# Kernel tuning notes

Hardware: AMD Instinct MI355X
Metric: run time of the kernel (lower is better)

Reference implementation:

```python
import jax, jax.numpy as jnp
import numpy as np

USERNUM = 100_000
ITEMNUM = 50_000
EMBED_DIM = 64
N_INTERACTIONS = 2_000_000
NUM_LAYERS = 3
BATCH = 4096


def setup_inputs() -> dict:
    rng = np.random.default_rng(0)
    # random bipartite interactions: users 1..USERNUM, items 1..ITEMNUM
    u = rng.integers(1, USERNUM + 1, N_INTERACTIONS)
    it = rng.integers(1, ITEMNUM + 1, N_INTERACTIONS)
    # node ids: user k -> k, item j -> USERNUM + j (matches build_graph)
    rows = np.concatenate([u, USERNUM + it]).astype(np.int32)
    cols = np.concatenate([USERNUM + it, u]).astype(np.int32)
    n_nodes = USERNUM + ITEMNUM + 1
    # symmetric normalization D^-1/2 A D^-1/2 (duplicate edges sum, as in scipy COO)
    deg = np.bincount(rows, minlength=n_nodes).astype(np.float32)
    d_inv_sqrt = np.where(deg > 0, deg ** -0.5, 0.0).astype(np.float32)
    vals = (d_inv_sqrt[rows] * d_inv_sqrt[cols]).astype(np.float32)

    key = jax.random.key(0)
    k1, k2, k3, k4, k5 = jax.random.split(key, 5)
    # xavier_normal init: std = sqrt(2 / (fan_in + fan_out))
    u_std = np.sqrt(2.0 / (USERNUM + 1 + EMBED_DIM)).astype(np.float32)
    i_std = np.sqrt(2.0 / (ITEMNUM + 1 + EMBED_DIM)).astype(np.float32)
    user_table = jax.random.normal(k1, (USERNUM + 1, EMBED_DIM), jnp.float32) * u_std
    item_table = jax.random.normal(k2, (ITEMNUM + 1, EMBED_DIM), jnp.float32) * i_std

    user_ids = jax.random.randint(k3, (BATCH,), 0, USERNUM + 1)
    pos_seqs = jax.random.randint(k4, (BATCH,), 1, ITEMNUM + 1)
    neg_seqs = jax.random.randint(k5, (BATCH,), 1, ITEMNUM + 1)

    return {
        "user_table": user_table,
        "item_table": item_table,
        "vals": jnp.asarray(vals),
        "rows": jnp.asarray(rows),
        "cols": jnp.asarray(cols),
        "user_ids": user_ids,
        "pos_seqs": pos_seqs,
        "neg_seqs": neg_seqs,
    }


def reference(user_table, item_table, vals, rows, cols, user_ids, pos_seqs, neg_seqs):
    usernum = user_table.shape[0] - 1
    itemnum = item_table.shape[0] - 1
    n_nodes = usernum + itemnum + 1

    # ego embeddings: users 0..usernum, items 1..itemnum (skip item padding row)
    x = jnp.concatenate([user_table, item_table[1:]], axis=0)  # [n_nodes, D]

    # LightGCN propagation: x_{l+1} = A_norm @ x_l (SpMM via gather + segment_sum),
    # layer combination = mean over layers 0..NUM_LAYERS
    acc = x
    for _ in range(NUM_LAYERS):
        msgs = vals[:, None] * x[cols]              # [nnz, D]
        x = jax.ops.segment_sum(msgs, rows, num_segments=n_nodes)
        acc = acc + x
    all_emb = acc / (NUM_LAYERS + 1)

    uidx = jnp.clip(user_ids, 0, usernum)
    pidx = usernum + jnp.clip(pos_seqs, 1, itemnum)  # item j lives at row usernum + j
    nidx = usernum + jnp.clip(neg_seqs, 1, itemnum)

    u_emb = all_emb[uidx]
    pos_logits = jnp.sum(u_emb * all_emb[pidx], axis=-1)
    neg_logits = jnp.sum(u_emb * all_emb[nidx], axis=-1)
    return pos_logits, neg_logits
```

## Files before the change

### kernel.cpp

```cpp
#include <hip/hip_runtime.h>
#include <hip/hip_fp16.h>
#include <cstdint>
#include <cstddef>


typedef __attribute__((ext_vector_type(8))) _Float16 half8;

#define NB_SHIFT 8
#define BCAP 16000
#define P1_SRC 4096
#define P1_DIM 512

__global__ __launch_bounds__(P1_DIM) void partition_kernel(
    const int* __restrict__ rows, const int* __restrict__ cols,
    int* __restrict__ bucket_cursor, int* __restrict__ tmp,
    int M , int nb) {
    __shared__ int            lhist[1024];
    __shared__ int            loff[1024];
    __shared__ int            ldelta[1024];
    __shared__ int            wsum[8];
    __shared__ int            stage[2 * P1_SRC];
    __shared__ unsigned short bstage[2 * P1_SRC];
    int t = threadIdx.x;
    int lane = t & 63, wv = t >> 6;
    int base     = blockIdx.x * P1_SRC;
    int cnt_here = min(P1_SRC, M - base);
    int full4    = cnt_here >> 2;
    int rem      = cnt_here & 3;
    for (int i = t; i < 1024; i += P1_DIM) lhist[i] = 0;
    __syncthreads();
    const int4* rows4 = (const int4*)(rows + base);
    const int4* cols4 = (const int4*)(cols + base);
    int4 uu[2], vv[2];
    int  rka[8], rkb[8];
#pragma unroll
    for (int k = 0; k < 2; ++k) {
        int i4 = t + k * P1_DIM;
        if (i4 < full4) {
            uu[k] = rows4[i4];
            vv[k] = cols4[i4];
            int u4[4] = {uu[k].x, uu[k].y, uu[k].z, uu[k].w};
            int v4[4] = {vv[k].x, vv[k].y, vv[k].z, vv[k].w};
#pragma unroll
            for (int e = 0; e < 4; ++e) {
                rka[4 * k + e] = atomicAdd(&lhist[u4[e] >> NB_SHIFT], 1);
                rkb[4 * k + e] = atomicAdd(&lhist[v4[e] >> NB_SHIFT], 1);
            }
        }
    }
    int ur = 0, vr = 0, rkra = 0, rkrb = 0;
    bool has_rem = (t < rem);
    if (has_rem) {
        ur = rows[base + 4 * full4 + t];
        vr = cols[base + 4 * full4 + t];
        rkra = atomicAdd(&lhist[ur >> NB_SHIFT], 1);
        rkrb = atomicAdd(&lhist[vr >> NB_SHIFT], 1);
    }
    __syncthreads();
    int v0 = lhist[2 * t], v1 = lhist[2 * t + 1];
    int ts = v0 + v1;
    int sc = ts;
#pragma unroll
    for (int off = 1; off < 64; off <<= 1) {
        int x = __shfl_up(sc, off);
        if (lane >= off) sc += x;
    }
    if (lane == 63) wsum[wv] = sc;
    __syncthreads();
    int prefix = 0;
#pragma unroll
    for (int k = 0; k < 8; ++k) {
        int s = wsum[k];
        prefix += (k < wv) ? s : 0;
    }
    int run = prefix + sc - ts;
    loff[2 * t]     = run;
    loff[2 * t + 1] = run + v0;
#pragma unroll
    for (int k = 0; k < 2; ++k) {
        int b  = 2 * t + k;
        int vvk = (k == 0) ? v0 : v1;
        if (b < nb && vvk > 0) {
            int old = atomicAdd(&bucket_cursor[b], vvk);
            ldelta[b] = b * BCAP + old - loff[b];
        }
    }
    __syncthreads();
#pragma unroll
    for (int k = 0; k < 2; ++k) {
        int i4 = t + k * P1_DIM;
        if (i4 < full4) {
            int u4[4] = {uu[k].x, uu[k].y, uu[k].z, uu[k].w};
            int v4[4] = {vv[k].x, vv[k].y, vv[k].z, vv[k].w};
#pragma unroll
            for (int e = 0; e < 4; ++e) {
                int ub = u4[e] >> NB_SHIFT;
                int s1 = loff[ub] + rka[4 * k + e];
                stage[s1]  = ((u4[e] & 255) << 18) | v4[e];
                bstage[s1] = (unsigned short)ub;
                int vb = v4[e] >> NB_SHIFT;
                int s2 = loff[vb] + rkb[4 * k + e];
                stage[s2]  = ((v4[e] & 255) << 18) | u4[e];
                bstage[s2] = (unsigned short)vb;
            }
        }
    }
    if (has_rem) {
        int ub = ur >> NB_SHIFT;
        int s1 = loff[ub] + rkra;
        stage[s1]  = ((ur & 255) << 18) | vr;
        bstage[s1] = (unsigned short)ub;
        int vb = vr >> NB_SHIFT;
        int s2 = loff[vb] + rkrb;
        stage[s2]  = ((vr & 255) << 18) | ur;
        bstage[s2] = (unsigned short)vb;
    }
    __syncthreads();
    int total = 2 * cnt_here;
    for (int s = t; s < total; s += P1_DIM) {
        tmp[s + ldelta[bstage[s]]] = stage[s];
    }
}

__global__ __launch_bounds__(256) void finalize_kernel(
    const int* __restrict__ tmp, const int* __restrict__ bcur,
    const float4* __restrict__ ut4, const float4* __restrict__ it4,
    int* __restrict__ row_ptr, float* __restrict__ dis,
    float* __restrict__ dis2, float* __restrict__ invd,
    int* __restrict__ cv, half8* __restrict__ Yh0,
    int usernum, int n_nodes, int nb, int nnz) {
    __shared__ int   rcnt[256];
    __shared__ int   ccur[256];
    __shared__ int   wsum[4];
    __shared__ int   red[256];
    __shared__ float sdis[256];
    int b = blockIdx.x;
    int t = threadIdx.x;
    int lane = t & 63, wv = t >> 6;
    int partial = 0;
    for (int i = t; i < nb; i += 256) {
        int c = bcur[i];
        if (i < b) partial += c;
    }
    red[t] = partial;
    __syncthreads();
    for (int off = 128; off > 0; off >>= 1) {
        if (t < off) red[t] += red[t + off];
        __syncthreads();
    }
    int dbeg  = red[0];
    int count = bcur[b];
    int src   = b * BCAP;
    rcnt[t] = 0;
    __syncthreads();
    for (int i = t; i < count; i += 256) {
        atomicAdd(&rcnt[tmp[src + i] >> 18], 1);
    }
    __syncthreads();
    int v = rcnt[t];
    int sc = v;
#pragma unroll
    for (int off = 1; off < 64; off <<= 1) {
        int x = __shfl_up(sc, off);
        if (lane >= off) sc += x;
    }
    if (lane == 63) wsum[wv] = sc;
    __syncthreads();
    int prefix = 0;
#pragma unroll
    for (int k = 0; k < 4; ++k) {
        int s = wsum[k];
        prefix += (k < wv) ? s : 0;
    }
    int ex = prefix + sc - v;
    ccur[t] = ex;
    int row = (b << NB_SHIFT) + t;
    float dval = 0.0f;
    if (row < n_nodes) {
        row_ptr[row] = dbeg + ex;
        double dv = (double)v;
        dval      = (v > 0) ? (float)(1.0 / sqrt(dv)) : 0.0f;
        dis[row]  = dval;
        dis2[row] = (v > 0) ? (float)(1.0 / dv) : 0.0f;
        invd[row] = (v > 0) ? (float)sqrt(dv) : 0.0f;
    }
    sdis[t] = dval;
    if (b == nb - 1 && t == 0) row_ptr[n_nodes] = nnz;
    __syncthreads();
    for (int i = t; i < count; i += 256) {
        int p  = tmp[src + i];
        int rk = atomicAdd(&ccur[p >> 18], 1);
        cv[dbeg + rk] = p & 0x3FFFF;
    }
    int row0 = b << NB_SHIFT;
    for (int i = t; i < 256 * 8; i += 256) {
        int rl = i >> 3;
        int rg = row0 + rl;
        if (rg < n_nodes) {
            int c = i & 7;
            float d = sdis[rl];
            const float4* srcp = (rg <= usernum)
                ? (ut4 + (size_t)rg * 16 + 2 * c)
                : (it4 + (size_t)(rg - usernum) * 16 + 2 * c);
            float4 a = srcp[0];
            float4 e = srcp[1];
            half8 o;
            o[0] = (_Float16)(d * a.x); o[1] = (_Float16)(d * a.y);
            o[2] = (_Float16)(d * a.z); o[3] = (_Float16)(d * a.w);
            o[4] = (_Float16)(d * e.x); o[5] = (_Float16)(d * e.y);
            o[6] = (_Float16)(d * e.z); o[7] = (_Float16)(d * e.w);
            Yh0[(size_t)rg * 8 + c] = o;
        }
    }
}

__device__ inline float csr_row_sum_h(const _Float16* __restrict__ Yh,
                                      const int* __restrict__ cv,
                                      int beg, int end, int g, int l8,
                                      float one) {
    float acc[8] = {0.f, 0.f, 0.f, 0.f, 0.f, 0.f, 0.f, 0.f};
    const char* Yb = (const char*)Yh;
    const char* cb = (const char*)cv;
    unsigned lo = (unsigned)l8 * 16u;
    int j = beg + g;
    for (; j + 8 < end; j += 16) {
        unsigned c0 = (unsigned)*(const int*)(cb + ((unsigned)j << 2));
        unsigned c1 = (unsigned)*(const int*)(cb + ((unsigned)(j + 8) << 2));
        half8 x0 = *(const half8*)(Yb + (c0 << 7) + lo);
        half8 x1 = *(const half8*)(Yb + (c1 << 7) + lo);
        half8 tt = x0 + x1;
#pragma unroll
        for (int k = 0; k < 8; ++k) {
            acc[k] += one * (float)tt[k];
        }
    }
    if (j < end) {
        unsigned c0 = (unsigned)*(const int*)(cb + ((unsigned)j << 2));
        half8 x0 = *(const half8*)(Yb + (c0 << 7) + lo);
#pragma unroll
        for (int k = 0; k < 8; ++k) {
            acc[k] += one * (float)x0[k];
        }
    }
    bool gb0 = (g & 1) != 0;
    bool gb1 = (g & 2) != 0;
    bool gb2 = (g & 4) != 0;
    float s0 = gb0 ? acc[0] : acc[4];
    float s1 = gb0 ? acc[1] : acc[5];
    float s2 = gb0 ? acc[2] : acc[6];
    float s3 = gb0 ? acc[3] : acc[7];
    float a0 = (gb0 ? acc[4] : acc[0]) + __shfl_xor(s0, 8);
    float a1 = (gb0 ? acc[5] : acc[1]) + __shfl_xor(s1, 8);
    float a2 = (gb0 ? acc[6] : acc[2]) + __shfl_xor(s2, 8);
    float a3 = (gb0 ? acc[7] : acc[3]) + __shfl_xor(s3, 8);
    float t0 = gb1 ? a0 : a2;
    float t1 = gb1 ? a1 : a3;
    float b0 = (gb1 ? a2 : a0) + __shfl_xor(t0, 16);
    float b1 = (gb1 ? a3 : a1) + __shfl_xor(t1, 16);
    float u = gb2 ? b0 : b1;
    float fin = (gb2 ? b1 : b0) + __shfl_xor(u, 32);
    return fin;
}

__device__ inline int lane_dim(int g, int l8) {
    return l8 * 8 + ((g & 1) * 4 + (g & 2) + (g >> 2));
}

__global__ __launch_bounds__(256) void spmm_y_kernel(
    const _Float16* __restrict__ Yin, _Float16* __restrict__ Yout,
    const int* __restrict__ row_ptr, const int* __restrict__ cv,
    const float* __restrict__ dis2, float one, int n_nodes) {
    int wid  = (blockIdx.x * blockDim.x + threadIdx.x) >> 6;
    int lane = threadIdx.x & 63;
    int g = lane >> 3, sub = lane & 7;
    int row = wid * 8 + g;
    bool ok = row < n_nodes;
    int beg = 0, end = 0;
    if (ok) {
        beg = row_ptr[row];
        end = row_ptr[row + 1];
    }
    float d2 = ok ? dis2[row] : 0.0f;
    const char* Yb = (const char*)Yin;
    const char* cb = (const char*)cv;
    unsigned lo = (unsigned)sub * 16u;
    float acc[8] = {0.f, 0.f, 0.f, 0.f, 0.f, 0.f, 0.f, 0.f};
    int len = end - beg;
    int mx = len;
    mx = max(mx, __shfl_xor(mx, 8));
    mx = max(mx, __shfl_xor(mx, 16));
    mx = max(mx, __shfl_xor(mx, 32));
    int iters = (mx + 7) >> 3;
    int j = beg;
    size_t jb = ((size_t)(unsigned)j) << 2;
    int r0 = *(const int*)(cb + jb);
    int r1 = *(const int*)(cb + jb + 4u);
    int r2 = *(const int*)(cb + jb + 8u);
    int r3 = *(const int*)(cb + jb + 12u);
    int r4 = *(const int*)(cb + jb + 16u);
    int r5 = *(const int*)(cb + jb + 20u);
    int r6 = *(const int*)(cb + jb + 24u);
    int r7 = *(const int*)(cb + jb + 28u);
    for (int it = 0; it < iters; ++it) {
        unsigned c0 = (unsigned)((j     < end) ? r0 : 0);
        unsigned c1 = (unsigned)((j + 1 < end) ? r1 : 0);
        unsigned c2 = (unsigned)((j + 2 < end) ? r2 : 0);
        unsigned c3 = (unsigned)((j + 3 < end) ? r3 : 0);
        unsigned c4 = (unsigned)((j + 4 < end) ? r4 : 0);
        unsigned c5 = (unsigned)((j + 5 < end) ? r5 : 0);
        unsigned c6 = (unsigned)((j + 6 < end) ? r6 : 0);
        unsigned c7 = (unsigned)((j + 7 < end) ? r7 : 0);
        half8 x0 = *(const half8*)(Yb + ((size_t)c0 << 7) + lo);
        half8 x1 = *(const half8*)(Yb + ((size_t)c1 << 7) + lo);
        half8 x2 = *(const half8*)(Yb + ((size_t)c2 << 7) + lo);
        half8 x3 = *(const half8*)(Yb + ((size_t)c3 << 7) + lo);
        half8 x4 = *(const half8*)(Yb + ((size_t)c4 << 7) + lo);
        half8 x5 = *(const half8*)(Yb + ((size_t)c5 << 7) + lo);
        half8 x6 = *(const half8*)(Yb + ((size_t)c6 << 7) + lo);
        half8 x7 = *(const half8*)(Yb + ((size_t)c7 << 7) + lo);
        j += 8;
        jb = ((size_t)(unsigned)j) << 2;
        r0 = *(const int*)(cb + jb);
        r1 = *(const int*)(cb + jb + 4u);
        r2 = *(const int*)(cb + jb + 8u);
        r3 = *(const int*)(cb + jb + 12u);
        r4 = *(const int*)(cb + jb + 16u);
        r5 = *(const int*)(cb + jb + 20u);
        r6 = *(const int*)(cb + jb + 24u);
        r7 = *(const int*)(cb + jb + 28u);
        half8 sA = (x0 + x1) + (x2 + x3);
        half8 sB = (x4 + x5) + (x6 + x7);
        half8 tt = sA + sB;
#pragma unroll
        for (int k = 0; k < 8; ++k) {
            acc[k] += one * (float)tt[k];
        }
    }
    if (ok) {
        half8 o;
#pragma unroll
        for (int k = 0; k < 8; ++k) o[k] = (_Float16)(acc[k] * d2);
        *(half8*)((char*)Yout + ((size_t)row << 7) + lo) = o;
    }
}

__global__ __launch_bounds__(256) void gather_logits_kernel(
    const float* __restrict__ ut, const float* __restrict__ itb,
    const _Float16* __restrict__ Y1, const _Float16* __restrict__ Y2,
    const int* __restrict__ row_ptr, const int* __restrict__ cv,
    const float* __restrict__ dis, const float* __restrict__ invd,
    const int* __restrict__ user_ids, const int* __restrict__ pos_seqs,
    const int* __restrict__ neg_seqs, float* __restrict__ out,
    float one, int usernum, int itemnum, int batch) {
    int w    = (blockIdx.x * blockDim.x + threadIdx.x) >> 6;
    int lane = threadIdx.x & 63;
    if (w >= batch) return;
    int g = lane >> 3, l8 = lane & 7;
    int d = lane_dim(g, l8);
    int idxs[3];
    int u = min(max(user_ids[w], 0), usernum);
    idxs[0] = u;
    int p = min(max(pos_seqs[w], 1), itemnum);
    idxs[1] = usernum + p;
    int nn = min(max(neg_seqs[w], 1), itemnum);
    idxs[2] = usernum + nn;
    float vals[3];
#pragma unroll
    for (int q = 0; q < 3; ++q) {
        int idx = idxs[q];
        int beg = row_ptr[idx];
        int end = row_ptr[idx + 1];
        float dr = dis[idx];
        float iv = invd[idx];
        float fin = csr_row_sum_h(Y2, cv, beg, end, g, l8, one);
        const float* base0 = (q == 0) ? (ut + (size_t)u * 64)
                                      : (itb + (size_t)(idx - usernum) * 64);
        float x0v = base0[d];
        float y1v = (float)Y1[(size_t)idx * 64 + d];
        float y2v = (float)Y2[(size_t)idx * 64 + d];
        vals[q] = x0v + iv * (y1v + y2v) + fin * dr;
    }
    float dp = vals[0] * vals[1];
    float dn = vals[0] * vals[2];
#pragma unroll
    for (int off = 1; off < 64; off <<= 1) {
        dp += __shfl_xor(dp, off);
        dn += __shfl_xor(dn, off);
    }
    if (lane == 0) {
        out[w]         = dp * 0.0625f;
        out[batch + w] = dn * 0.0625f;
    }
}

extern "C" void kernel_launch(void* const* d_in, const int* in_sizes, int n_in,
                              void* d_out, int out_size, void* d_ws,
                              size_t ws_size, hipStream_t stream) {
    const float* user_table = (const float*)d_in[0];
    const float* item_table = (const float*)d_in[1];
    const int*   rows       = (const int*)d_in[3];
    const int*   cols       = (const int*)d_in[4];
    const int*   user_ids   = (const int*)d_in[5];
    const int*   pos_seqs   = (const int*)d_in[6];
    const int*   neg_seqs   = (const int*)d_in[7];
    float*       out        = (float*)d_out;

    const int D = 64;
    int usernum = in_sizes[0] / D - 1;
    int itemnum = in_sizes[1] / D - 1;
    int nnz     = in_sizes[2];
    int batch   = in_sizes[5];
    int n_nodes = usernum + itemnum + 1;
    int nb      = (n_nodes + (1 << NB_SHIFT) - 1) >> NB_SHIFT;
    int M       = nnz >> 1;

    char* w = (char*)d_ws;
    auto alloc = [&](size_t bytes) {
        char* p = w;
        w += (bytes + 255) & ~(size_t)255;
        return p;
    };
    _Float16* Yh0   = (_Float16*)alloc((size_t)n_nodes * D * 2);
    _Float16* Yh1   = (_Float16*)alloc((size_t)n_nodes * D * 2);
    _Float16* Yh2   = (_Float16*)alloc((size_t)n_nodes * D * 2);
    int*   cv       = (int*)alloc((size_t)nnz * 4 + 8192);
    int*   row_ptr  = (int*)alloc((size_t)(n_nodes + 1) * 4);
    float* dis      = (float*)alloc((size_t)n_nodes * 4);
    float* dis2     = (float*)alloc((size_t)n_nodes * 4);
    float* invd     = (float*)alloc((size_t)n_nodes * 4);
    int*   bcur     = (int*)alloc(4096);
    int*   tmp      = (int*)Yh1;

    hipMemsetAsync(bcur, 0, 4096, stream);
    int p1_tiles = (M + P1_SRC - 1) / P1_SRC;
    partition_kernel<<<p1_tiles, P1_DIM, 0, stream>>>(rows, cols, bcur, tmp,
                                                      M, nb);
    finalize_kernel<<<nb, 256, 0, stream>>>(
        tmp, bcur, (const float4*)user_table, (const float4*)item_table,
        row_ptr, dis, dis2, invd, cv, (half8*)Yh0, usernum, n_nodes, nb, nnz);

    const float one = 1.0f;
    int spmm_grid = (n_nodes + 31) / 32;
    spmm_y_kernel<<<spmm_grid, 256, 0, stream>>>(Yh0, Yh1, row_ptr, cv, dis2,
                                                 one, n_nodes);
    spmm_y_kernel<<<spmm_grid, 256, 0, stream>>>(Yh1, Yh2, row_ptr, cv, dis2,
                                                 one, n_nodes);

    gather_logits_kernel<<<(batch + 3) / 4, 256, 0, stream>>>(
        user_table, item_table, Yh1, Yh2, row_ptr, cv, dis, invd, user_ids,
        pos_seqs, neg_seqs, out, one, usernum, itemnum, batch);
}
```

Baseline: 303.0 us.

## Split Y0 conversion out of finalize and widen finalize blocks to 512

Moves the scaled fp16 conversion of the ego embeddings out of the CSR finalize kernel into its own fully parallel kernel, so it no longer runs at low parallelism inside the roughly 590 finalize blocks. Finalize now uses 512 threads per block for the bucket counting and scatter loops and only sums the preceding bucket counts. The cursor now carries the global offset directly. The cost is an extra kernel launch and a re-read of dis from global memory.

```diff
diff --git a/kernel.cpp b/kernel.cpp
--- a/kernel.cpp
+++ b/kernel.cpp
@@ -122,96 +122,94 @@
     }
 }
 
-__global__ __launch_bounds__(256) void finalize_kernel(
+__global__ __launch_bounds__(512) void finalize_kernel(
     const int* __restrict__ tmp, const int* __restrict__ bcur,
-    const float4* __restrict__ ut4, const float4* __restrict__ it4,
     int* __restrict__ row_ptr, float* __restrict__ dis,
     float* __restrict__ dis2, float* __restrict__ invd,
-    int* __restrict__ cv, half8* __restrict__ Yh0,
-    int usernum, int n_nodes, int nb, int nnz) {
-    __shared__ int   rcnt[256];
-    __shared__ int   ccur[256];
-    __shared__ int   wsum[4];
-    __shared__ int   red[256];
-    __shared__ float sdis[256];
+    int* __restrict__ cv, int n_nodes, int nb, int nnz) {
+    __shared__ int rcnt[256];
+    __shared__ int ccur[256];
+    __shared__ int wsum[4];
+    __shared__ int red[512];
     int b = blockIdx.x;
     int t = threadIdx.x;
     int lane = t & 63, wv = t >> 6;
     int partial = 0;
-    for (int i = t; i < nb; i += 256) {
-        int c = bcur[i];
-        if (i < b) partial += c;
-    }
+    for (int i = t; i < b; i += 512) partial += bcur[i];
     red[t] = partial;
     __syncthreads();
-    for (int off = 128; off > 0; off >>= 1) {
+    for (int off = 256; off > 0; off >>= 1) {
         if (t < off) red[t] += red[t + off];
         __syncthreads();
     }
     int dbeg  = red[0];
     int count = bcur[b];
     int src   = b * BCAP;
-    rcnt[t] = 0;
-    __syncthreads();
-    for (int i = t; i < count; i += 256) {
+    if (t < 256) rcnt[t] = 0;
+    __syncthreads();
+    for (int i = t; i < count; i += 512) {
         atomicAdd(&rcnt[tmp[src + i] >> 18], 1);
     }
     __syncthreads();
-    int v = rcnt[t];
-    int sc = v;
-#pragma unroll
-    for (int off = 1; off < 64; off <<= 1) {
-        int x = __shfl_up(sc, off);
-        if (lane >= off) sc += x;
-    }
-    if (lane == 63) wsum[wv] = sc;
-    __syncthreads();
-    int prefix = 0;
-#pragma unroll
-    for (int k = 0; k < 4; ++k) {
-        int s = wsum[k];
-        prefix += (k < wv) ? s : 0;
-    }
-    int ex = prefix + sc - v;
-    ccur[t] = ex;
-    int row = (b << NB_SHIFT) + t;
-    float dval = 0.0f;
-    if (row < n_nodes) {
-        row_ptr[row] = dbeg + ex;
-        double dv = (double)v;
-        dval      = (v > 0) ? (float)(1.0 / sqrt(dv)) : 0.0f;
-        dis[row]  = dval;
-        dis2[row] = (v > 0) ? (float)(1.0 / dv) : 0.0f;
-        invd[row] = (v > 0) ? (float)sqrt(dv) : 0.0f;
-    }
-    sdis[t] = dval;
+    int v = 0, sc = 0;
+    if (t < 256) {
+        v  = rcnt[t];
+        sc = v;
+#pragma unroll
+        for (int off = 1; off < 64; off <<= 1) {
+            int x = __shfl_up(sc, off);
+            if (lane >= off) sc += x;
+        }
+        if (lane == 63) wsum[wv] = sc;
+    }
+    __syncthreads();
+    if (t < 256) {
+        int prefix = 0;
+#pragma unroll
+        for (int k = 0; k < 4; ++k) {
+            int s = wsum[k];
+            prefix += (k < wv) ? s : 0;
+        }
+        int ex = prefix + sc - v;
+        ccur[t] = dbeg + ex;
+        int row = (b << NB_SHIFT) + t;
+        if (row < n_nodes) {
+            row_ptr[row] = dbeg + ex;
+            double dv = (double)v;
+            dis[row]  = (v > 0) ? (float)(1.0 / sqrt(dv)) : 0.0f;
+            dis2[row] = (v > 0) ? (float)(1.0 / dv) : 0.0f;
+            invd[row] = (v > 0) ? (float)sqrt(dv) : 0.0f;
+        }
+    }
     if (b == nb - 1 && t == 0) row_ptr[n_nodes] = nnz;
     __syncthreads();
-    for (int i = t; i < count; i += 256) {
+    for (int i = t; i < count; i += 512) {
         int p  = tmp[src + i];
         int rk = atomicAdd(&ccur[p >> 18], 1);
-        cv[dbeg + rk] = p & 0x3FFFF;
-    }
-    int row0 = b << NB_SHIFT;
-    for (int i = t; i < 256 * 8; i += 256) {
-        int rl = i >> 3;
-        int rg = row0 + rl;
-        if (rg < n_nodes) {
-            int c = i & 7;
-            float d = sdis[rl];
-            const float4* srcp = (rg <= usernum)
-                ? (ut4 + (size_t)rg * 16 + 2 * c)
-                : (it4 + (size_t)(rg - usernum) * 16 + 2 * c);
-            float4 a = srcp[0];
-            float4 e = srcp[1];
-            half8 o;
-            o[0] = (_Float16)(d * a.x); o[1] = (_Float16)(d * a.y);
-            o[2] = (_Float16)(d * a.z); o[3] = (_Float16)(d * a.w);
-            o[4] = (_Float16)(d * e.x); o[5] = (_Float16)(d * e.y);
-            o[6] = (_Float16)(d * e.z); o[7] = (_Float16)(d * e.w);
-            Yh0[(size_t)rg * 8 + c] = o;
-        }
-    }
+        cv[rk] = p & 0x3FFFF;
+    }
+}
+
+__global__ __launch_bounds__(256) void convert_y0_kernel(
+    const float4* __restrict__ ut4, const float4* __restrict__ it4,
+    const float* __restrict__ dis, half8* __restrict__ Yh0,
+    int usernum, int n_nodes) {
+    int idx = blockIdx.x * 256 + threadIdx.x;
+    int row = idx >> 3;
+    if (row >= n_nodes) return;
+    int c = idx & 7;
+    float d = dis[row];
+    const float4* srcp = (row <= usernum)
+        ? (ut4 + (size_t)row * 16 + 2 * c)
+        : (it4 + (size_t)(row - usernum) * 16 + 2 * c);
+    float4 a = srcp[0];
+    float4 e = srcp[1];
+    half8 o;
+    o[0] = (_Float16)(d * a.x); o[1] = (_Float16)(d * a.y);
+    o[2] = (_Float16)(d * a.z); o[3] = (_Float16)(d * a.w);
+    o[4] = (_Float16)(d * e.x); o[5] = (_Float16)(d * e.y);
+    o[6] = (_Float16)(d * e.z); o[7] = (_Float16)(d * e.w);
+    Yh0[(size_t)row * 8 + c] = o;
 }
 
 __device__ inline float csr_row_sum_h(const _Float16* __restrict__ Yh,
@@ -435,9 +433,12 @@
     int p1_tiles = (M + P1_SRC - 1) / P1_SRC;
     partition_kernel<<<p1_tiles, P1_DIM, 0, stream>>>(rows, cols, bcur, tmp,
                                                       M, nb);
-    finalize_kernel<<<nb, 256, 0, stream>>>(
-        tmp, bcur, (const float4*)user_table, (const float4*)item_table,
-        row_ptr, dis, dis2, invd, cv, (half8*)Yh0, usernum, n_nodes, nb, nnz);
+    finalize_kernel<<<nb, 512, 0, stream>>>(tmp, bcur, row_ptr, dis, dis2,
+                                            invd, cv, n_nodes, nb, nnz);
+    int conv_blocks = (n_nodes * 8 + 255) / 256;
+    convert_y0_kernel<<<conv_blocks, 256, 0, stream>>>(
+        (const float4*)user_table, (const float4*)item_table, dis,
+        (half8*)Yh0, usernum, n_nodes);
 
     const float one = 1.0f;
     int spmm_grid = (n_nodes + 31) / 32;
```

Result: faster. 292.4 us (-3.5%).
